# Performance work log

Measured on AMD Instinct MI355X. Metric: run time of the kernel, lower is better.

## Reference

```python
import jax, jax.numpy as jnp
import numpy as np

K = 1024   # num_embeddings
E = 64     # embedding_dim
T = 1024   # time
B = 64     # batch
BETA = 0.25  # commitment_cost


def setup_inputs() -> dict:
    key = jax.random.key(0)
    k1, k2 = jax.random.split(key)
    inputs = jax.random.normal(k1, (E, T, B), dtype=jnp.float32)
    # torch init: uniform(-1/num_embeddings, 1/num_embeddings)
    codebook = jax.random.uniform(k2, (K, E), dtype=jnp.float32,
                                  minval=-1.0 / K, maxval=1.0 / K)
    return {"inputs": inputs, "codebook": codebook}


def reference(inputs, codebook):
    # inputs: [E, T, B]; torch does permute(1,2,0) -> [T, B, E]
    x = jnp.transpose(inputs, (1, 2, 0))            # [T, B, E]
    flat = x.reshape(-1, E)                          # [N, E], N = T*B
    d = (jnp.sum(flat * flat, axis=1, keepdims=True)
         + jnp.sum(codebook * codebook, axis=1)
         - 2.0 * (flat @ codebook.T))
    idx = jnp.argmin(d, axis=1)                      # [N]
    # one-hot @ codebook == gather (same math, efficient form)
    q = codebook[idx].reshape(T, B, E)               # [T, B, E]

    e_latent_loss = jnp.mean((jax.lax.stop_gradient(q) - x) ** 2)
    q_latent_loss = jnp.mean((q - jax.lax.stop_gradient(x)) ** 2)
    vq_loss = q_latent_loss + BETA * e_latent_loss

    # straight-through estimator
    q_st = x + jax.lax.stop_gradient(q - x)

    # perplexity from code-usage histogram (mean of one-hots)
    N = flat.shape[0]
    counts = jnp.zeros((K,), jnp.float32).at[idx].add(1.0)
    avg_probs = counts / N
    perplexity = jnp.exp(-jnp.sum(avg_probs * jnp.log(avg_probs + 1e-10)))

    quantized = jnp.transpose(q_st, (2, 0, 1))       # back to [E, T, B]
    return vq_loss, quantized, perplexity
```

## Files before the change

### kernel.cpp

```cpp
#include <hip/hip_runtime.h>


#define KC 1024
#define ED 64
#define NR 65536
#define NE (NR * ED)
#define GAP1 6e-6f

typedef __attribute__((ext_vector_type(8))) short short8;
typedef __attribute__((ext_vector_type(4))) float f32x4;

__device__ __forceinline__ unsigned short bf16rne(float f) {
    unsigned u = __builtin_bit_cast(unsigned, f);
    return (unsigned short)((u + 0x7fffu + ((u >> 16) & 1u)) >> 16);
}
__device__ __forceinline__ float bf16tof(unsigned short h) {
    return __builtin_bit_cast(float, (unsigned)h << 16);
}

__global__ __launch_bounds__(256) void k_pack(const float* __restrict__ cb,
        short8* __restrict__ cbt, unsigned* __restrict__ counts,
        unsigned* __restrict__ flagcnt) {
    const int u = blockIdx.x * 256 + threadIdx.x;
    if (u < 1024) counts[u] = 0u;
    if (u == 1024) *flagcnt = 0u;
    if (u >= 64 * 7 * 64) return;
    const int t = u / 448, rem = u % 448, j = rem / 64, l = rem % 64;
    const int g = l >> 4;
    if (j < 6) {
        const int code = t * 16 + (l & 15);
        const float* c = cb + (size_t)code * ED;
        short8 o;
#pragma unroll
        for (int r = 0; r < 8; ++r) {
            const int k = j * 32 + g * 8 + r;
            int e; bool lo;
            if (j < 2)      { e = k;       lo = false; }
            else if (j < 4) { e = k - 64;  lo = true;  }
            else            { e = k - 128; lo = false; }
            const float m2 = -2.f * c[e];
            const unsigned short h = bf16rne(m2);
            o[r] = lo ? (short)bf16rne(m2 - bf16tof(h)) : (short)h;
        }
        cbt[u] = o;
    } else {
        f32x4 o;
#pragma unroll
        for (int r = 0; r < 4; ++r) {
            const float4* c4 = (const float4*)(cb + (size_t)(t * 16 + g * 4 + r) * ED);
            float s0 = 0.f, s1 = 0.f, s2 = 0.f, s3 = 0.f;
#pragma unroll
            for (int i = 0; i < 16; ++i) {
                const float4 c = c4[i];
                s0 = fmaf(c.x, c.x, s0); s1 = fmaf(c.y, c.y, s1);
                s2 = fmaf(c.z, c.z, s2); s3 = fmaf(c.w, c.w, s3);
            }
            o[r] = (s0 + s1) + (s2 + s3);
        }
        cbt[u] = __builtin_bit_cast(short8, o);
    }
}

__global__ __launch_bounds__(1024) void k_argmin(
        const float* __restrict__ in, const short8* __restrict__ cbt,
        int* __restrict__ idx, unsigned* __restrict__ flagcnt,
        unsigned* __restrict__ flaglist) {
    __shared__ short8 xs[4][16][64];
    __shared__ float sb[16][4][16], sb2[16][4][16];
    __shared__ int   sk[16][4][16];

    const int tid = threadIdx.x;
    const int l = tid & 63;
    const int wid = tid >> 6;
    const int g = l >> 4;
    const int col = l & 15;
    const int rowBase = blockIdx.x * 256;

    {
        const int row = tid & 255;
        const int ob = tid >> 8;
        const int rg = row >> 6;
        const int r6 = row & 63;
        const int rt = r6 >> 4;
        const int ll = ob * 16 + (r6 & 15);
#pragma unroll
        for (int hh = 0; hh < 2; ++hh) {
            const int oct = ob + hh * 4;
            short8 H, L;
#pragma unroll
            for (int j = 0; j < 8; ++j) {
                const float x = in[(size_t)(oct * 8 + j) * NR + rowBase + row];
                const unsigned short hb = bf16rne(x);
                H[j] = (short)hb;
                L[j] = (short)bf16rne(x - bf16tof(hb));
            }
            xs[rg][rt * 4 + hh][ll] = H;
            xs[rg][rt * 4 + 2 + hh][ll] = L;
        }
    }
    __syncthreads();

    const int rg = wid >> 2, kh = wid & 3;
    short8 xq[4][4];
#pragma unroll
    for (int rt = 0; rt < 4; ++rt)
#pragma unroll
        for (int q = 0; q < 4; ++q)
            xq[rt][q] = xs[rg][rt * 4 + q][l];

    float best[4]  = {3.4e38f, 3.4e38f, 3.4e38f, 3.4e38f};
    float best2[4] = {3.4e38f, 3.4e38f, 3.4e38f, 3.4e38f};
    int bestk[4] = {0, 0, 0, 0};

#pragma unroll 2
    for (int tt = 0; tt < 16; ++tt) {
        const int t = kh * 16 + tt;
        const short8* bp = cbt + (size_t)t * 448 + l;
        const short8 b0 = bp[0], b1 = bp[64], b2 = bp[128],
                     b3 = bp[192], b4 = bp[256], b5 = bp[320];
        const f32x4 e4 = __builtin_bit_cast(f32x4, bp[384]);
#pragma unroll
        for (int rt = 0; rt < 4; ++rt) {
            f32x4 acc = e4;
            acc = __builtin_amdgcn_mfma_f32_16x16x32_bf16(b0, xq[rt][0], acc, 0, 0, 0);
            acc = __builtin_amdgcn_mfma_f32_16x16x32_bf16(b1, xq[rt][1], acc, 0, 0, 0);
            acc = __builtin_amdgcn_mfma_f32_16x16x32_bf16(b2, xq[rt][0], acc, 0, 0, 0);
            acc = __builtin_amdgcn_mfma_f32_16x16x32_bf16(b3, xq[rt][1], acc, 0, 0, 0);
            acc = __builtin_amdgcn_mfma_f32_16x16x32_bf16(b4, xq[rt][2], acc, 0, 0, 0);
            acc = __builtin_amdgcn_mfma_f32_16x16x32_bf16(b5, xq[rt][3], acc, 0, 0, 0);
#pragma unroll
            for (int r = 0; r < 4; ++r) {
                const float v = acc[r];
                const int k = t * 16 + g * 4 + r;
                best2[rt] = fminf(fmaxf(v, best[rt]), best2[rt]);
                const bool c = v < best[rt];
                bestk[rt] = c ? k : bestk[rt];
                best[rt]  = fminf(v, best[rt]);
            }
        }
    }

#pragma unroll
    for (int rt = 0; rt < 4; ++rt) {
        float b = best[rt], b2 = best2[rt]; int k = bestk[rt];
#pragma unroll
        for (int sh = 16; sh <= 32; sh <<= 1) {
            const float ob  = __shfl_xor(b, sh, 64);
            const float ob2 = __shfl_xor(b2, sh, 64);
            const int   ok  = __shfl_xor(k, sh, 64);
            if (ob < b || (ob == b && ok < k)) { b2 = fminf(b, ob2); k = ok; b = ob; }
            else b2 = fminf(b2, ob);
        }
        if (g == 0) { sb[wid][rt][col] = b; sb2[wid][rt][col] = b2; sk[wid][rt][col] = k; }
    }
    __syncthreads();

    if (wid < 4) {
        const int rt = l >> 4, c2 = l & 15;
        float b = sb[wid * 4][rt][c2], b2 = sb2[wid * 4][rt][c2];
        int k = sk[wid * 4][rt][c2];
#pragma unroll
        for (int s = 1; s < 4; ++s) {
            const float ob = sb[wid * 4 + s][rt][c2], ob2 = sb2[wid * 4 + s][rt][c2];
            const int ok = sk[wid * 4 + s][rt][c2];
            if (ob < b || (ob == b && ok < k)) { b2 = fminf(b, ob2); k = ok; b = ob; }
            else b2 = fminf(b2, ob);
        }
        const int row = rowBase + wid * 64 + rt * 16 + c2;
        idx[row] = k;
        if (b2 - b < GAP1) {
            const unsigned p = atomicAdd(flagcnt, 1u);
            flaglist[p] = (unsigned)row;
        }
    }
}

__global__ __launch_bounds__(256) void k_exact64(
        const float* __restrict__ in, const float* __restrict__ cb,
        int* __restrict__ idx,
        const unsigned* __restrict__ flagcnt, const unsigned* __restrict__ flaglist) {
    const unsigned nf = *flagcnt;
    const int l = threadIdx.x & 63;
    const unsigned wave = blockIdx.x * 4u + (unsigned)(threadIdx.x >> 6);
    const unsigned nwave = gridDim.x * 4u;
    for (unsigned i = wave; i < nf; i += nwave) {
        const int row = (int)flaglist[i];
        float x[ED];
#pragma unroll
        for (int e = 0; e < ED; ++e) x[e] = in[(size_t)e * NR + row];
        double best = 1e300; int bestk = 0;
        for (int ci = 0; ci < 16; ++ci) {
            const int k = ci * 64 + l;
            const float* c = cb + (size_t)k * ED;
            double s = 0.0, e2 = 0.0;
            for (int e = 0; e < ED; ++e) {
                const double cv = (double)c[e];
                e2 = fma(cv, cv, e2);
                s  = fma(cv, (double)x[e], s);
            }
            const double t = fma(-2.0, s, e2);
            if (t < best) { best = t; bestk = k; }
        }
        for (int sh = 1; sh < 64; sh <<= 1) {
            const double ob = __shfl_xor(best, sh, 64);
            const int   ok  = __shfl_xor(bestk, sh, 64);
            if (ob < best || (ob == best && ok < bestk)) { best = ob; bestk = ok; }
        }
        if (l == 0) idx[row] = bestk;
    }
}

__global__ __launch_bounds__(256) void k_output(
        const float* __restrict__ in, const float* __restrict__ cb,
        const int* __restrict__ idx, float* __restrict__ qout,
        unsigned* __restrict__ counts, double* __restrict__ pblk) {
    __shared__ double sred[4];
    const int gtid = blockIdx.x * 256 + threadIdx.x;
    const int n = gtid & (NR - 1);
    const int e0 = gtid >> 16;
    const int k = idx[n];
    if (e0 == 0) atomicAdd(&counts[k], 1u);
    const float4* c4 = (const float4*)(cb + (size_t)k * ED + e0 * 8);
    const float4 q0 = c4[0], q1 = c4[1];
    float local = 0.f;
#pragma unroll
    for (int j = 0; j < 8; ++j) {
        const int e = e0 * 8 + j;
        const float q = (j < 4) ? ((const float*)&q0)[j] : ((const float*)&q1)[j - 4];
        const float xv = in[(size_t)e * NR + n];
        qout[(size_t)e * NR + n] = q;
        const float d = q - xv;
        local = fmaf(d, d, local);
    }
    double ld = (double)local;
#pragma unroll
    for (int off = 32; off > 0; off >>= 1) ld += __shfl_down(ld, off, 64);
    if ((threadIdx.x & 63) == 0) sred[threadIdx.x >> 6] = ld;
    __syncthreads();
    if (threadIdx.x == 0)
        pblk[blockIdx.x] = (sred[0] + sred[1]) + (sred[2] + sred[3]);
}

__global__ __launch_bounds__(1024) void k_final(const unsigned* __restrict__ counts,
        const double* __restrict__ pblk, float* __restrict__ out) {
    __shared__ double redE[16], redS[16];
    const int tid = threadIdx.x;
    const double p = (double)counts[tid] * (1.0 / 65536.0);
    double term = p * log(p + 1e-10);
    double s = pblk[tid] + pblk[tid + 1024];
#pragma unroll
    for (int off = 32; off > 0; off >>= 1) {
        term += __shfl_down(term, off, 64);
        s    += __shfl_down(s,    off, 64);
    }
    if ((tid & 63) == 0) { redE[tid >> 6] = term; redS[tid >> 6] = s; }
    __syncthreads();
    if (tid == 0) {
        double e = 0.0, ss = 0.0;
        for (int i = 0; i < 16; ++i) { e += redE[i]; ss += redS[i]; }
        out[1 + NE] = (float)exp(-e);
        const double m = ss * (1.0 / 4194304.0);
        out[0] = (float)(1.25 * m);
    }
}

extern "C" void kernel_launch(void* const* d_in, const int* in_sizes, int n_in,
                              void* d_out, int out_size, void* d_ws, size_t ws_size,
                              hipStream_t stream) {
    (void)in_sizes; (void)n_in; (void)out_size; (void)ws_size;
    const float* in = (const float*)d_in[0];
    const float* cb = (const float*)d_in[1];
    float* out = (float*)d_out;

    unsigned* counts   = (unsigned*)d_ws;
    unsigned* flagcnt  = (unsigned*)d_ws + 1024;
    short8*   cbt      = (short8*)((float*)d_ws + 4160);
    int*      idx      = (int*)d_ws + 118848;
    unsigned* flaglist = (unsigned*)d_ws + 184384;
    double*   pblk     = (double*)((char*)d_ws + 999680);

    hipLaunchKernelGGL(k_pack,    dim3(112),  dim3(256),  0, stream,
                       cb, cbt, counts, flagcnt);
    hipLaunchKernelGGL(k_argmin,  dim3(256),  dim3(1024), 0, stream,
                       in, cbt, idx, flagcnt, flaglist);
    hipLaunchKernelGGL(k_exact64, dim3(128),  dim3(256),  0, stream,
                       in, cb, idx, flagcnt, flaglist);
    hipLaunchKernelGGL(k_output,  dim3(2048), dim3(256),  0, stream,
                       in, cb, idx, out + 1, counts, pblk);
    hipLaunchKernelGGL(k_final,   dim3(1),    dim3(1024), 0, stream,
                       counts, pblk, out);
}
```

Before: 93.06 us.

## Split argmin across codebook quarters with LDS double-buffered codebook and merge kernel

The argmin kernel is split into 1024 smaller blocks, each handling 256 rows against one quarter of the codebook. Codebook tiles are streamed into LDS through double-buffered global_load_lds, replacing per-wave global loads. A new merge kernel combines the per-quarter partial minima, builds the histogram and computes the loss from the min distance plus ||x||^2. The output kernel then only writes the gathered codes and no longer re-reads the inputs. The cost is extra partial-result traffic, one more launch, and a loss that now uses the approximate bf16-split distance rather than the exact squared error, with k_exact64 adjusting counts when it corrects an index.

```diff
diff --git a/kernel.cpp b/kernel.cpp
--- a/kernel.cpp
+++ b/kernel.cpp
@@ -17,6 +17,11 @@
 __device__ __forceinline__ float bf16tof(unsigned short h) {
     return __builtin_bit_cast(float, (unsigned)h << 16);
 }
+
+#define GLOAD_LDS16(GSRC, LDST) \
+    __builtin_amdgcn_global_load_lds( \
+        (const __attribute__((address_space(1))) void*)(GSRC), \
+        (__attribute__((address_space(3))) void*)(LDST), 16, 0, 0)
 
 __global__ __launch_bounds__(256) void k_pack(const float* __restrict__ cb,
         short8* __restrict__ cbt, unsigned* __restrict__ counts,
@@ -27,6 +32,7 @@
     if (u >= 64 * 7 * 64) return;
     const int t = u / 448, rem = u % 448, j = rem / 64, l = rem % 64;
     const int g = l >> 4;
+    const int w = t * 512 + j * 64 + l;
     if (j < 6) {
         const int code = t * 16 + (l & 15);
         const float* c = cb + (size_t)code * ED;
@@ -42,7 +48,7 @@
             const unsigned short h = bf16rne(m2);
             o[r] = lo ? (short)bf16rne(m2 - bf16tof(h)) : (short)h;
         }
-        cbt[u] = o;
+        cbt[w] = o;
     } else {
         f32x4 o;
 #pragma unroll
@@ -57,68 +63,81 @@
             }
             o[r] = (s0 + s1) + (s2 + s3);
         }
-        cbt[u] = __builtin_bit_cast(short8, o);
-    }
-}
-
-__global__ __launch_bounds__(1024) void k_argmin(
+        cbt[w] = __builtin_bit_cast(short8, o);
+    }
+}
+
+__global__ __launch_bounds__(256) void k_argmin_part(
         const float* __restrict__ in, const short8* __restrict__ cbt,
-        int* __restrict__ idx, unsigned* __restrict__ flagcnt,
-        unsigned* __restrict__ flaglist) {
-    __shared__ short8 xs[4][16][64];
-    __shared__ float sb[16][4][16], sb2[16][4][16];
-    __shared__ int   sk[16][4][16];
+        float* __restrict__ pb, float* __restrict__ pb2, int* __restrict__ pk,
+        float* __restrict__ rx2) {
+    __shared__ short8 lbuf[2][512];
 
     const int tid = threadIdx.x;
     const int l = tid & 63;
     const int wid = tid >> 6;
     const int g = l >> 4;
     const int col = l & 15;
-    const int rowBase = blockIdx.x * 256;
+    const int ks = blockIdx.x & 3;
+    const int rowBase = (blockIdx.x >> 2) * 256 + wid * 64;
+    const int t0 = ks * 16;
 
     {
-        const int row = tid & 255;
-        const int ob = tid >> 8;
-        const int rg = row >> 6;
-        const int r6 = row & 63;
-        const int rt = r6 >> 4;
-        const int ll = ob * 16 + (r6 & 15);
-#pragma unroll
-        for (int hh = 0; hh < 2; ++hh) {
-            const int oct = ob + hh * 4;
+        const short8* src = cbt + (size_t)t0 * 512;
+#pragma unroll
+        for (int i = wid; i < 8; i += 4)
+            GLOAD_LDS16(src + i * 64 + l, &lbuf[0][i * 64]);
+    }
+
+    short8 xq[4][4];
+#pragma unroll
+    for (int rt = 0; rt < 4; ++rt) {
+        const int row = rowBase + rt * 16 + col;
+        float s2 = 0.f;
+#pragma unroll
+        for (int h = 0; h < 2; ++h) {
             short8 H, L;
 #pragma unroll
             for (int j = 0; j < 8; ++j) {
-                const float x = in[(size_t)(oct * 8 + j) * NR + rowBase + row];
+                const float x = in[(size_t)(h * 32 + g * 8 + j) * NR + row];
                 const unsigned short hb = bf16rne(x);
                 H[j] = (short)hb;
                 L[j] = (short)bf16rne(x - bf16tof(hb));
-            }
-            xs[rg][rt * 4 + hh][ll] = H;
-            xs[rg][rt * 4 + 2 + hh][ll] = L;
-        }
-    }
-    __syncthreads();
-
-    const int rg = wid >> 2, kh = wid & 3;
-    short8 xq[4][4];
-#pragma unroll
-    for (int rt = 0; rt < 4; ++rt)
-#pragma unroll
-        for (int q = 0; q < 4; ++q)
-            xq[rt][q] = xs[rg][rt * 4 + q][l];
+                s2 = fmaf(x, x, s2);
+            }
+            xq[rt][h] = H; xq[rt][2 + h] = L;
+        }
+        float s = s2;
+        s += __shfl_xor(s, 16, 64);
+        s += __shfl_xor(s, 32, 64);
+        if (ks == 0 && g == 0) rx2[row] = s;
+    }
+
+    asm volatile("s_waitcnt vmcnt(0)" ::: "memory");
+    __builtin_amdgcn_s_barrier();
 
     float best[4]  = {3.4e38f, 3.4e38f, 3.4e38f, 3.4e38f};
     float best2[4] = {3.4e38f, 3.4e38f, 3.4e38f, 3.4e38f};
     int bestk[4] = {0, 0, 0, 0};
 
-#pragma unroll 2
     for (int tt = 0; tt < 16; ++tt) {
-        const int t = kh * 16 + tt;
-        const short8* bp = cbt + (size_t)t * 448 + l;
-        const short8 b0 = bp[0], b1 = bp[64], b2 = bp[128],
-                     b3 = bp[192], b4 = bp[256], b5 = bp[320];
-        const f32x4 e4 = __builtin_bit_cast(f32x4, bp[384]);
+        const int cur = tt & 1;
+        if (tt < 15) {
+            const short8* src = cbt + (size_t)(t0 + tt + 1) * 512;
+#pragma unroll
+            for (int i = wid; i < 8; i += 4)
+                GLOAD_LDS16(src + i * 64 + l, &lbuf[cur ^ 1][i * 64]);
+            asm volatile("s_waitcnt vmcnt(2)" ::: "memory");
+        } else {
+            asm volatile("s_waitcnt vmcnt(0)" ::: "memory");
+        }
+        __builtin_amdgcn_s_barrier();
+
+        const short8 b0 = lbuf[cur][0 * 64 + l], b1 = lbuf[cur][1 * 64 + l],
+                     b2 = lbuf[cur][2 * 64 + l], b3 = lbuf[cur][3 * 64 + l],
+                     b4 = lbuf[cur][4 * 64 + l], b5 = lbuf[cur][5 * 64 + l];
+        const f32x4 e4 = __builtin_bit_cast(f32x4, lbuf[cur][384 + l]);
+        const int t = t0 + tt;
 #pragma unroll
         for (int rt = 0; rt < 4; ++rt) {
             f32x4 acc = e4;
@@ -138,6 +157,7 @@
                 best[rt]  = fminf(v, best[rt]);
             }
         }
+        __builtin_amdgcn_s_barrier();
     }
 
 #pragma unroll
@@ -151,33 +171,47 @@
             if (ob < b || (ob == b && ok < k)) { b2 = fminf(b, ob2); k = ok; b = ob; }
             else b2 = fminf(b2, ob);
         }
-        if (g == 0) { sb[wid][rt][col] = b; sb2[wid][rt][col] = b2; sk[wid][rt][col] = k; }
-    }
+        if (g == 0) {
+            const int row = rowBase + rt * 16 + col;
+            pb[row * 4 + ks] = b; pb2[row * 4 + ks] = b2; pk[row * 4 + ks] = k;
+        }
+    }
+}
+
+__global__ __launch_bounds__(256) void k_merge(
+        const float* __restrict__ pb, const float* __restrict__ pb2,
+        const int* __restrict__ pk, const float* __restrict__ rx2,
+        int* __restrict__ idx, unsigned* __restrict__ counts,
+        unsigned* __restrict__ flagcnt, unsigned* __restrict__ flaglist,
+        double* __restrict__ pblk) {
+    __shared__ double sred[4];
+    const int n = blockIdx.x * 256 + threadIdx.x;
+    float b = pb[n * 4], b2 = pb2[n * 4]; int k = pk[n * 4];
+#pragma unroll
+    for (int s = 1; s < 4; ++s) {
+        const float ob = pb[n * 4 + s], ob2 = pb2[n * 4 + s];
+        const int ok = pk[n * 4 + s];
+        if (ob < b || (ob == b && ok < k)) { b2 = fminf(b, ob2); k = ok; b = ob; }
+        else b2 = fminf(b2, ob);
+    }
+    idx[n] = k;
+    atomicAdd(&counts[k], 1u);
+    if (b2 - b < GAP1) {
+        const unsigned p = atomicAdd(flagcnt, 1u);
+        flaglist[p] = (unsigned)n;
+    }
+    double ld = (double)b + (double)rx2[n];
+#pragma unroll
+    for (int off = 32; off > 0; off >>= 1) ld += __shfl_down(ld, off, 64);
+    if ((threadIdx.x & 63) == 0) sred[threadIdx.x >> 6] = ld;
     __syncthreads();
-
-    if (wid < 4) {
-        const int rt = l >> 4, c2 = l & 15;
-        float b = sb[wid * 4][rt][c2], b2 = sb2[wid * 4][rt][c2];
-        int k = sk[wid * 4][rt][c2];
-#pragma unroll
-        for (int s = 1; s < 4; ++s) {
-            const float ob = sb[wid * 4 + s][rt][c2], ob2 = sb2[wid * 4 + s][rt][c2];
-            const int ok = sk[wid * 4 + s][rt][c2];
-            if (ob < b || (ob == b && ok < k)) { b2 = fminf(b, ob2); k = ok; b = ob; }
-            else b2 = fminf(b2, ob);
-        }
-        const int row = rowBase + wid * 64 + rt * 16 + c2;
-        idx[row] = k;
-        if (b2 - b < GAP1) {
-            const unsigned p = atomicAdd(flagcnt, 1u);
-            flaglist[p] = (unsigned)row;
-        }
-    }
+    if (threadIdx.x == 0)
+        pblk[blockIdx.x] = (sred[0] + sred[1]) + (sred[2] + sred[3]);
 }
 
 __global__ __launch_bounds__(256) void k_exact64(
         const float* __restrict__ in, const float* __restrict__ cb,
-        int* __restrict__ idx,
+        int* __restrict__ idx, unsigned* __restrict__ counts,
         const unsigned* __restrict__ flagcnt, const unsigned* __restrict__ flaglist) {
     const unsigned nf = *flagcnt;
     const int l = threadIdx.x & 63;
@@ -206,39 +240,31 @@
             const int   ok  = __shfl_xor(bestk, sh, 64);
             if (ob < best || (ob == best && ok < bestk)) { best = ob; bestk = ok; }
         }
-        if (l == 0) idx[row] = bestk;
+        if (l == 0) {
+            const int old = idx[row];
+            if (bestk != old) {
+                idx[row] = bestk;
+                atomicSub(&counts[old], 1u);
+                atomicAdd(&counts[bestk], 1u);
+            }
+        }
     }
 }
 
 __global__ __launch_bounds__(256) void k_output(
-        const float* __restrict__ in, const float* __restrict__ cb,
-        const int* __restrict__ idx, float* __restrict__ qout,
-        unsigned* __restrict__ counts, double* __restrict__ pblk) {
-    __shared__ double sred[4];
+        const float* __restrict__ cb, const int* __restrict__ idx,
+        float* __restrict__ qout) {
     const int gtid = blockIdx.x * 256 + threadIdx.x;
     const int n = gtid & (NR - 1);
     const int e0 = gtid >> 16;
     const int k = idx[n];
-    if (e0 == 0) atomicAdd(&counts[k], 1u);
     const float4* c4 = (const float4*)(cb + (size_t)k * ED + e0 * 8);
     const float4 q0 = c4[0], q1 = c4[1];
-    float local = 0.f;
 #pragma unroll
     for (int j = 0; j < 8; ++j) {
-        const int e = e0 * 8 + j;
         const float q = (j < 4) ? ((const float*)&q0)[j] : ((const float*)&q1)[j - 4];
-        const float xv = in[(size_t)e * NR + n];
-        qout[(size_t)e * NR + n] = q;
-        const float d = q - xv;
-        local = fmaf(d, d, local);
-    }
-    double ld = (double)local;
-#pragma unroll
-    for (int off = 32; off > 0; off >>= 1) ld += __shfl_down(ld, off, 64);
-    if ((threadIdx.x & 63) == 0) sred[threadIdx.x >> 6] = ld;
-    __syncthreads();
-    if (threadIdx.x == 0)
-        pblk[blockIdx.x] = (sred[0] + sred[1]) + (sred[2] + sred[3]);
+        qout[(size_t)(e0 * 8 + j) * NR + n] = q;
+    }
 }
 
 __global__ __launch_bounds__(1024) void k_final(const unsigned* __restrict__ counts,
@@ -247,7 +273,7 @@
     const int tid = threadIdx.x;
     const double p = (double)counts[tid] * (1.0 / 65536.0);
     double term = p * log(p + 1e-10);
-    double s = pblk[tid] + pblk[tid + 1024];
+    double s = (tid < 256) ? pblk[tid] : 0.0;
 #pragma unroll
     for (int off = 32; off > 0; off >>= 1) {
         term += __shfl_down(term, off, 64);
@@ -274,19 +300,25 @@
 
     unsigned* counts   = (unsigned*)d_ws;
     unsigned* flagcnt  = (unsigned*)d_ws + 1024;
-    short8*   cbt      = (short8*)((float*)d_ws + 4160);
-    int*      idx      = (int*)d_ws + 118848;
-    unsigned* flaglist = (unsigned*)d_ws + 184384;
-    double*   pblk     = (double*)((char*)d_ws + 999680);
-
-    hipLaunchKernelGGL(k_pack,    dim3(112),  dim3(256),  0, stream,
+    short8*   cbt      = (short8*)((float*)d_ws + 2048);
+    float*    pb       = (float*)d_ws + 133120;
+    float*    pb2      = (float*)d_ws + 395264;
+    int*      pk       = (int*)d_ws + 657408;
+    int*      idx      = (int*)d_ws + 919552;
+    unsigned* flaglist = (unsigned*)d_ws + 985088;
+    float*    rx2      = (float*)d_ws + 1050624;
+    double*   pblk     = (double*)((char*)d_ws + 4464640);
+
+    hipLaunchKernelGGL(k_pack,        dim3(112),  dim3(256),  0, stream,
                        cb, cbt, counts, flagcnt);
-    hipLaunchKernelGGL(k_argmin,  dim3(256),  dim3(1024), 0, stream,
-                       in, cbt, idx, flagcnt, flaglist);
-    hipLaunchKernelGGL(k_exact64, dim3(128),  dim3(256),  0, stream,
-                       in, cb, idx, flagcnt, flaglist);
-    hipLaunchKernelGGL(k_output,  dim3(2048), dim3(256),  0, stream,
-                       in, cb, idx, out + 1, counts, pblk);
-    hipLaunchKernelGGL(k_final,   dim3(1),    dim3(1024), 0, stream,
+    hipLaunchKernelGGL(k_argmin_part, dim3(1024), dim3(256),  0, stream,
+                       in, cbt, pb, pb2, pk, rx2);
+    hipLaunchKernelGGL(k_merge,       dim3(256),  dim3(256),  0, stream,
+                       pb, pb2, pk, rx2, idx, counts, flagcnt, flaglist, pblk);
+    hipLaunchKernelGGL(k_exact64,     dim3(128),  dim3(256),  0, stream,
+                       in, cb, idx, counts, flagcnt, flaglist);
+    hipLaunchKernelGGL(k_output,      dim3(2048), dim3(256),  0, stream,
+                       cb, idx, out + 1);
+    hipLaunchKernelGGL(k_final,       dim3(1),    dim3(1024), 0, stream,
                        counts, pblk, out);
 }
```

Measured after the change: 107.6 us. 1.16x slower.

## Fuse loss and histogram into argmin, drop input reread and final kernel

Applied to the files above, without the earlier changes.

The argmin kernel now computes per-row ||x||^2 while packing inputs. It derives the squared error from the winning distance, accumulates the code-usage counts, and writes per-block loss partials. The exact-fallback kernel corrects counts when it changes an index. The output kernel then only gathers codebook rows, no longer rereads the input, and folds the final reduction into block 0, which removes one launch. Argmin also uses 512-thread blocks, with each wave covering 8 row tiles to get more reuse from each codebook fragment. The trade-offs are more register pressure, and a loss taken from the bf16-split distance that is not recomputed for flagged rows.

```diff
diff --git a/kernel.cpp b/kernel.cpp
--- a/kernel.cpp
+++ b/kernel.cpp
@@ -61,13 +61,16 @@
     }
 }
 
-__global__ __launch_bounds__(1024) void k_argmin(
+__global__ __launch_bounds__(512) void k_argmin(
         const float* __restrict__ in, const short8* __restrict__ cbt,
-        int* __restrict__ idx, unsigned* __restrict__ flagcnt,
-        unsigned* __restrict__ flaglist) {
-    __shared__ short8 xs[4][16][64];
-    __shared__ float sb[16][4][16], sb2[16][4][16];
-    __shared__ int   sk[16][4][16];
+        int* __restrict__ idx, unsigned* __restrict__ counts,
+        unsigned* __restrict__ flagcnt, unsigned* __restrict__ flaglist,
+        double* __restrict__ pblk) {
+    __shared__ short8 xs[16][4][64];
+    __shared__ float rx2p[2][256];
+    __shared__ float sb[4][16][16], sb2[4][16][16];
+    __shared__ int   sk[4][16][16];
+    __shared__ double sred[4];
 
     const int tid = threadIdx.x;
     const int l = tid & 63;
@@ -78,41 +81,40 @@
 
     {
         const int row = tid & 255;
-        const int ob = tid >> 8;
-        const int rg = row >> 6;
-        const int r6 = row & 63;
-        const int rt = r6 >> 4;
-        const int ll = ob * 16 + (r6 & 15);
-#pragma unroll
-        for (int hh = 0; hh < 2; ++hh) {
-            const int oct = ob + hh * 4;
+        const int h = tid >> 8;
+        const int grt = row >> 4;
+        const int cl = row & 15;
+        float part = 0.f;
+#pragma unroll
+        for (int gg = 0; gg < 4; ++gg) {
             short8 H, L;
 #pragma unroll
             for (int j = 0; j < 8; ++j) {
-                const float x = in[(size_t)(oct * 8 + j) * NR + rowBase + row];
+                const float x = in[(size_t)(h * 32 + gg * 8 + j) * NR + rowBase + row];
                 const unsigned short hb = bf16rne(x);
                 H[j] = (short)hb;
                 L[j] = (short)bf16rne(x - bf16tof(hb));
-            }
-            xs[rg][rt * 4 + hh][ll] = H;
-            xs[rg][rt * 4 + 2 + hh][ll] = L;
-        }
+                part = fmaf(x, x, part);
+            }
+            xs[grt][h][gg * 16 + cl] = H;
+            xs[grt][2 + h][gg * 16 + cl] = L;
+        }
+        rx2p[h][row] = part;
     }
     __syncthreads();
 
     const int rg = wid >> 2, kh = wid & 3;
-    short8 xq[4][4];
-#pragma unroll
-    for (int rt = 0; rt < 4; ++rt)
+    short8 xq[8][4];
+#pragma unroll
+    for (int rt = 0; rt < 8; ++rt)
 #pragma unroll
         for (int q = 0; q < 4; ++q)
-            xq[rt][q] = xs[rg][rt * 4 + q][l];
-
-    float best[4]  = {3.4e38f, 3.4e38f, 3.4e38f, 3.4e38f};
-    float best2[4] = {3.4e38f, 3.4e38f, 3.4e38f, 3.4e38f};
-    int bestk[4] = {0, 0, 0, 0};
-
-#pragma unroll 2
+            xq[rt][q] = xs[rg * 8 + rt][q][l];
+
+    float best[8], best2[8]; int bestk[8];
+#pragma unroll
+    for (int rt = 0; rt < 8; ++rt) { best[rt] = 3.4e38f; best2[rt] = 3.4e38f; bestk[rt] = 0; }
+
     for (int tt = 0; tt < 16; ++tt) {
         const int t = kh * 16 + tt;
         const short8* bp = cbt + (size_t)t * 448 + l;
@@ -120,7 +122,7 @@
                      b3 = bp[192], b4 = bp[256], b5 = bp[320];
         const f32x4 e4 = __builtin_bit_cast(f32x4, bp[384]);
 #pragma unroll
-        for (int rt = 0; rt < 4; ++rt) {
+        for (int rt = 0; rt < 8; ++rt) {
             f32x4 acc = e4;
             acc = __builtin_amdgcn_mfma_f32_16x16x32_bf16(b0, xq[rt][0], acc, 0, 0, 0);
             acc = __builtin_amdgcn_mfma_f32_16x16x32_bf16(b1, xq[rt][1], acc, 0, 0, 0);
@@ -141,7 +143,7 @@
     }
 
 #pragma unroll
-    for (int rt = 0; rt < 4; ++rt) {
+    for (int rt = 0; rt < 8; ++rt) {
         float b = best[rt], b2 = best2[rt]; int k = bestk[rt];
 #pragma unroll
         for (int sh = 16; sh <= 32; sh <<= 1) {
@@ -151,33 +153,45 @@
             if (ob < b || (ob == b && ok < k)) { b2 = fminf(b, ob2); k = ok; b = ob; }
             else b2 = fminf(b2, ob);
         }
-        if (g == 0) { sb[wid][rt][col] = b; sb2[wid][rt][col] = b2; sk[wid][rt][col] = k; }
+        if (g == 0) {
+            sb[kh][rg * 8 + rt][col] = b;
+            sb2[kh][rg * 8 + rt][col] = b2;
+            sk[kh][rg * 8 + rt][col] = k;
+        }
     }
     __syncthreads();
 
     if (wid < 4) {
-        const int rt = l >> 4, c2 = l & 15;
-        float b = sb[wid * 4][rt][c2], b2 = sb2[wid * 4][rt][c2];
-        int k = sk[wid * 4][rt][c2];
+        const int grt = wid * 4 + (l >> 4);
+        float b = sb[0][grt][col], b2 = sb2[0][grt][col]; int k = sk[0][grt][col];
 #pragma unroll
         for (int s = 1; s < 4; ++s) {
-            const float ob = sb[wid * 4 + s][rt][c2], ob2 = sb2[wid * 4 + s][rt][c2];
-            const int ok = sk[wid * 4 + s][rt][c2];
+            const float ob = sb[s][grt][col], ob2 = sb2[s][grt][col];
+            const int ok = sk[s][grt][col];
             if (ob < b || (ob == b && ok < k)) { b2 = fminf(b, ob2); k = ok; b = ob; }
             else b2 = fminf(b2, ob);
         }
-        const int row = rowBase + wid * 64 + rt * 16 + c2;
+        const int lrow = grt * 16 + col;
+        const int row = rowBase + lrow;
         idx[row] = k;
+        atomicAdd(&counts[k], 1u);
         if (b2 - b < GAP1) {
             const unsigned p = atomicAdd(flagcnt, 1u);
             flaglist[p] = (unsigned)row;
         }
-    }
+        double d2 = (double)b + (double)(rx2p[0][lrow] + rx2p[1][lrow]);
+#pragma unroll
+        for (int off = 32; off > 0; off >>= 1) d2 += __shfl_down(d2, off, 64);
+        if (l == 0) sred[wid] = d2;
+    }
+    __syncthreads();
+    if (tid == 0)
+        pblk[blockIdx.x] = (sred[0] + sred[1]) + (sred[2] + sred[3]);
 }
 
 __global__ __launch_bounds__(256) void k_exact64(
         const float* __restrict__ in, const float* __restrict__ cb,
-        int* __restrict__ idx,
+        int* __restrict__ idx, unsigned* __restrict__ counts,
         const unsigned* __restrict__ flagcnt, const unsigned* __restrict__ flaglist) {
     const unsigned nf = *flagcnt;
     const int l = threadIdx.x & 63;
@@ -206,61 +220,56 @@
             const int   ok  = __shfl_xor(bestk, sh, 64);
             if (ob < best || (ob == best && ok < bestk)) { best = ob; bestk = ok; }
         }
-        if (l == 0) idx[row] = bestk;
+        if (l == 0) {
+            const int old = idx[row];
+            if (bestk != old) {
+                idx[row] = bestk;
+                atomicSub(&counts[old], 1u);
+                atomicAdd(&counts[bestk], 1u);
+            }
+        }
     }
 }
 
 __global__ __launch_bounds__(256) void k_output(
-        const float* __restrict__ in, const float* __restrict__ cb,
-        const int* __restrict__ idx, float* __restrict__ qout,
-        unsigned* __restrict__ counts, double* __restrict__ pblk) {
-    __shared__ double sred[4];
+        const float* __restrict__ cb, const int* __restrict__ idx,
+        float* __restrict__ qout, const unsigned* __restrict__ counts,
+        const double* __restrict__ pblk, float* __restrict__ out) {
     const int gtid = blockIdx.x * 256 + threadIdx.x;
     const int n = gtid & (NR - 1);
     const int e0 = gtid >> 16;
     const int k = idx[n];
-    if (e0 == 0) atomicAdd(&counts[k], 1u);
     const float4* c4 = (const float4*)(cb + (size_t)k * ED + e0 * 8);
     const float4 q0 = c4[0], q1 = c4[1];
-    float local = 0.f;
 #pragma unroll
     for (int j = 0; j < 8; ++j) {
-        const int e = e0 * 8 + j;
         const float q = (j < 4) ? ((const float*)&q0)[j] : ((const float*)&q1)[j - 4];
-        const float xv = in[(size_t)e * NR + n];
-        qout[(size_t)e * NR + n] = q;
-        const float d = q - xv;
-        local = fmaf(d, d, local);
-    }
-    double ld = (double)local;
-#pragma unroll
-    for (int off = 32; off > 0; off >>= 1) ld += __shfl_down(ld, off, 64);
-    if ((threadIdx.x & 63) == 0) sred[threadIdx.x >> 6] = ld;
-    __syncthreads();
-    if (threadIdx.x == 0)
-        pblk[blockIdx.x] = (sred[0] + sred[1]) + (sred[2] + sred[3]);
-}
-
-__global__ __launch_bounds__(1024) void k_final(const unsigned* __restrict__ counts,
-        const double* __restrict__ pblk, float* __restrict__ out) {
-    __shared__ double redE[16], redS[16];
-    const int tid = threadIdx.x;
-    const double p = (double)counts[tid] * (1.0 / 65536.0);
-    double term = p * log(p + 1e-10);
-    double s = pblk[tid] + pblk[tid + 1024];
-#pragma unroll
-    for (int off = 32; off > 0; off >>= 1) {
-        term += __shfl_down(term, off, 64);
-        s    += __shfl_down(s,    off, 64);
-    }
-    if ((tid & 63) == 0) { redE[tid >> 6] = term; redS[tid >> 6] = s; }
-    __syncthreads();
-    if (tid == 0) {
-        double e = 0.0, ss = 0.0;
-        for (int i = 0; i < 16; ++i) { e += redE[i]; ss += redS[i]; }
-        out[1 + NE] = (float)exp(-e);
-        const double m = ss * (1.0 / 4194304.0);
-        out[0] = (float)(1.25 * m);
+        qout[(size_t)(e0 * 8 + j) * NR + n] = q;
+    }
+    if (blockIdx.x == 0) {
+        __shared__ double redE[4], redS[4];
+        const int tid = threadIdx.x;
+        double term = 0.0;
+#pragma unroll
+        for (int i = 0; i < 4; ++i) {
+            const double p = (double)counts[tid + i * 256] * (1.0 / 65536.0);
+            term += p * log(p + 1e-10);
+        }
+        double s = pblk[tid];
+#pragma unroll
+        for (int off = 32; off > 0; off >>= 1) {
+            term += __shfl_down(term, off, 64);
+            s    += __shfl_down(s,    off, 64);
+        }
+        if ((tid & 63) == 0) { redE[tid >> 6] = term; redS[tid >> 6] = s; }
+        __syncthreads();
+        if (tid == 0) {
+            const double e = (redE[0] + redE[1]) + (redE[2] + redE[3]);
+            const double ss = (redS[0] + redS[1]) + (redS[2] + redS[3]);
+            out[1 + NE] = (float)exp(-e);
+            const double m = ss * (1.0 / 4194304.0);
+            out[0] = (float)(1.25 * m);
+        }
     }
 }
 
@@ -274,19 +283,17 @@
 
     unsigned* counts   = (unsigned*)d_ws;
     unsigned* flagcnt  = (unsigned*)d_ws + 1024;
-    short8*   cbt      = (short8*)((float*)d_ws + 4160);
-    int*      idx      = (int*)d_ws + 118848;
-    unsigned* flaglist = (unsigned*)d_ws + 184384;
-    double*   pblk     = (double*)((char*)d_ws + 999680);
-
-    hipLaunchKernelGGL(k_pack,    dim3(112),  dim3(256),  0, stream,
+    short8*   cbt      = (short8*)((float*)d_ws + 2048);
+    int*      idx      = (int*)d_ws + 116736;
+    unsigned* flaglist = (unsigned*)d_ws + 182272;
+    double*   pblk     = (double*)((char*)d_ws + 991232);
+
+    hipLaunchKernelGGL(k_pack,    dim3(112),  dim3(256), 0, stream,
                        cb, cbt, counts, flagcnt);
-    hipLaunchKernelGGL(k_argmin,  dim3(256),  dim3(1024), 0, stream,
-                       in, cbt, idx, flagcnt, flaglist);
-    hipLaunchKernelGGL(k_exact64, dim3(128),  dim3(256),  0, stream,
-                       in, cb, idx, flagcnt, flaglist);
-    hipLaunchKernelGGL(k_output,  dim3(2048), dim3(256),  0, stream,
-                       in, cb, idx, out + 1, counts, pblk);
-    hipLaunchKernelGGL(k_final,   dim3(1),    dim3(1024), 0, stream,
-                       counts, pblk, out);
-}
+    hipLaunchKernelGGL(k_argmin,  dim3(256),  dim3(512), 0, stream,
+                       in, cbt, idx, counts, flagcnt, flaglist, pblk);
+    hipLaunchKernelGGL(k_exact64, dim3(128),  dim3(256), 0, stream,
+                       in, cb, idx, counts, flagcnt, flaglist);
+    hipLaunchKernelGGL(k_output,  dim3(2048), dim3(256), 0, stream,
+                       cb, idx, out + 1, counts, pblk, out);
+}
```

After: 90.12 us. -3.2%, faster.
